# Kernel tuning notes

Measured on AMD Instinct MI355X. Metric: run time of the kernel, lower is better.

The kernel has to match this reference:

```python
import jax, jax.numpy as jnp
import numpy as np

G, NPG = 8192, 8            # graphs, nodes per graph (8 sensors, recon head = 8*9)
N = G * NPG                 # 65536 total nodes
IN, HID, HEADS = 9, 64, 4
NEG_SLOPE = 0.2


def _fc_edges():
    # directed fully-connected edges (no self loops) within each 8-node graph
    i, j = np.meshgrid(np.arange(NPG), np.arange(NPG), indexing='ij')
    m = i != j
    src_l, dst_l = i[m], j[m]                       # 56 edges per graph
    off = (np.arange(G) * NPG)[:, None]
    src = (off + src_l[None, :]).ravel()
    dst = (off + dst_l[None, :]).ravel()
    return np.stack([src, dst]).astype(np.int32)    # [2, 458752]


def setup_inputs() -> dict:
    key = jax.random.key(0)
    ks = jax.random.split(key, 30)
    ei = jnp.asarray(_fc_edges())
    E = ei.shape[1]
    p = lambda k, shape, s=0.1: jax.random.normal(ks[k], shape, jnp.float32) * s
    return {
        'x': jax.random.normal(ks[0], (N, IN), jnp.float32),
        'edge_index': ei,
        'edge_weight': jax.random.uniform(ks[1], (E,), jnp.float32),
        'batch': jnp.repeat(jnp.arange(G, dtype=jnp.int32), NPG),
        'W1': p(2, (IN, HEADS * HID)), 'a_src1': p(3, (HEADS, HID)),
        'a_dst1': p(4, (HEADS, HID)), 'We1': p(5, (1, HEADS * HID)),
        'a_e1': p(6, (HEADS, HID)), 'b1': jnp.zeros((HEADS * HID,), jnp.float32),
        'W2': p(7, (HEADS * HID, HID)), 'a_src2': p(8, (1, HID)),
        'a_dst2': p(9, (1, HID)), 'We2': p(10, (1, HID)),
        'a_e2': p(11, (1, HID)), 'b2': jnp.zeros((HID,), jnp.float32),
        # recon head: 64 -> 128 -> 72
        'Wr1': p(12, (HID, 2 * HID)), 'br1': jnp.zeros((2 * HID,), jnp.float32),
        'Wr2': p(13, (2 * HID, 8 * IN)), 'br2': jnp.zeros((8 * IN,), jnp.float32),
        # classify head: 64 -> 32 -> 1
        'Wc1': p(14, (HID, 32)), 'bc1': jnp.zeros((32,), jnp.float32),
        'Wc2': p(15, (32, 1)), 'bc2': jnp.zeros((1,), jnp.float32),
    }


def _gat_conv(x, edge_index, edge_attr, W, a_src, a_dst, We, a_e, bias):
    """PyG GATConv (eval mode): add_self_loops(fill='mean'), edge_dim features."""
    n = x.shape[0]
    heads, ch = a_src.shape
    src, dst = edge_index[0], edge_index[1]
    # self loops with edge_attr = mean of incoming edge_attr per node
    deg = jax.ops.segment_sum(jnp.ones_like(edge_attr[:, :1]), dst, num_segments=n)
    loop_attr = jax.ops.segment_sum(edge_attr, dst, num_segments=n) / jnp.maximum(deg, 1.0)
    src = jnp.concatenate([src, jnp.arange(n, dtype=src.dtype)])
    dst = jnp.concatenate([dst, jnp.arange(n, dtype=dst.dtype)])
    ea = jnp.concatenate([edge_attr, loop_attr], axis=0)          # [E+N, 1]
    xp = (x @ W).reshape(n, heads, ch)                            # [N, H, C]
    al_s = jnp.einsum('nhc,hc->nh', xp, a_src)
    al_d = jnp.einsum('nhc,hc->nh', xp, a_dst)
    ep = (ea @ We).reshape(-1, heads, ch)                         # [E+N, H, C]
    al_e = jnp.einsum('ehc,hc->eh', ep, a_e)
    alpha = al_s[src] + al_d[dst] + al_e                          # [E+N, H]
    alpha = jax.nn.leaky_relu(alpha, NEG_SLOPE)
    # segment softmax over destination nodes
    m = jax.ops.segment_max(alpha, dst, num_segments=n)
    alpha = jnp.exp(alpha - m[dst])
    s = jax.ops.segment_sum(alpha, dst, num_segments=n)
    alpha = alpha / (s[dst] + 1e-16)
    # scatter-aggregate weighted messages
    out = jax.ops.segment_sum(xp[src] * alpha[..., None], dst, num_segments=n)
    return out.reshape(n, heads * ch) + bias


def reference(x, edge_index, edge_weight, batch,
              W1, a_src1, a_dst1, We1, a_e1, b1,
              W2, a_src2, a_dst2, We2, a_e2, b2,
              Wr1, br1, Wr2, br2, Wc1, bc1, Wc2, bc2):
    ew = edge_weight[:, None]
    h = _gat_conv(x, edge_index, ew, W1, a_src1, a_dst1, We1, a_e1, b1)
    h = jax.nn.elu(h)
    h = _gat_conv(h, edge_index, ew, W2, a_src2, a_dst2, We2, a_e2, b2)
    h = jax.nn.elu(h)
    # global mean pool over graphs
    g = G
    cnt = jax.ops.segment_sum(jnp.ones((h.shape[0], 1), h.dtype), batch, num_segments=g)
    emb = jax.ops.segment_sum(h, batch, num_segments=g) / jnp.maximum(cnt, 1.0)
    recon = jax.nn.relu(emb @ Wr1 + br1) @ Wr2 + br2
    cls = jax.nn.relu(emb @ Wc1 + bc1) @ Wc2 + bc2
    return recon, cls
```

## Files before the change

### kernel.cpp

```cpp
#include <hip/hip_runtime.h>
#include <math.h>

#define NEG 0.2f
#define GROUPS 8192

typedef unsigned short u16;
typedef u16 ushort8 __attribute__((ext_vector_type(8)));
typedef short s16x8 __attribute__((ext_vector_type(8)));
typedef float f32x4 __attribute__((ext_vector_type(4)));

__device__ __forceinline__ float lrelu(float x){ return x >= 0.f ? x : NEG*x; }
__device__ __forceinline__ float eluf(float x){ return x > 0.f ? x : __expf(x) - 1.f; }
__device__ __forceinline__ int eidx(int s,int d){ return s*7 + (d<s ? d : d-1); }
__device__ __forceinline__ float bf2f(u16 u){
    union { unsigned i; float f; } v; v.i = ((unsigned)u)<<16; return v.f;
}
__device__ __forceinline__ u16 f2bf(float f){
    union { float f; unsigned i; } v; v.f = f;
    unsigned r = v.i + 0x7fffu + ((v.i>>16)&1u);
    return (u16)(r>>16);
}

__global__ __launch_bounds__(64)
void prep(const float* __restrict__ W1, const float* __restrict__ a_src1,
          const float* __restrict__ a_dst1, const float* __restrict__ W2,
          const float* __restrict__ Wr1, const float* __restrict__ Wr2,
          const float* __restrict__ Wc1,
          const float* __restrict__ We1, const float* __restrict__ a_e1,
          const float* __restrict__ We2, const float* __restrict__ a_e2,
          u16* __restrict__ wfrag, u16* __restrict__ wr1f,
          u16* __restrict__ wr2f, u16* __restrict__ wc1f,
          float* __restrict__ w1s, float* __restrict__ ces)
{
    const int b = blockIdx.x, l = threadIdx.x;
    const int c0 = l & 15, o = l >> 4;
    if (b < 32) {
        const int t = b >> 3, s = b & 7;
        ushort8 p;
#pragma unroll
        for (int j = 0; j < 8; ++j) p[j] = f2bf(W2[(s*32 + o*8 + j)*64 + t*16 + c0]);
        *(ushort8*)(wfrag + (size_t)(b*64 + l)*8) = p;
    } else if (b < 48) {
        const int f = b - 32, ks = f >> 3, t = f & 7;
        ushort8 p;
#pragma unroll
        for (int j = 0; j < 8; ++j) p[j] = f2bf(Wr1[(ks*32 + o*8 + j)*128 + t*16 + c0]);
        *(ushort8*)(wr1f + (size_t)(f*64 + l)*8) = p;
    } else if (b < 68) {
        const int f = b - 48, ks = f / 5, t = f % 5;
        const int c = t*16 + c0;
        ushort8 p;
#pragma unroll
        for (int j = 0; j < 8; ++j)
            p[j] = (c < 72) ? f2bf(Wr2[(ks*32 + o*8 + j)*72 + c]) : (u16)0;
        *(ushort8*)(wr2f + (size_t)(f*64 + l)*8) = p;
    } else if (b < 72) {
        const int f = b - 68, ks = f >> 1, t = f & 1;
        ushort8 p;
#pragma unroll
        for (int j = 0; j < 8; ++j) p[j] = f2bf(Wc1[(ks*32 + o*8 + j)*32 + t*16 + c0]);
        *(ushort8*)(wc1f + (size_t)(f*64 + l)*8) = p;
    } else if (b == 72) {
        for (int idx = l; idx < 72; idx += 64) {
            const int k = idx >> 3, cc = idx & 7, h = cc & 3;
            const float* av = (cc < 4) ? a_src1 : a_dst1;
            float acc = 0.f;
#pragma unroll 8
            for (int i = 0; i < 64; ++i) acc = fmaf(W1[k*256 + h*64 + i], av[h*64 + i], acc);
            w1s[idx] = acc;
        }
    } else {
        if (l < 4) {
            float c = 0.f;
#pragma unroll 8
            for (int i = 0; i < 64; ++i) c = fmaf(We1[l*64+i], a_e1[l*64+i], c);
            ces[l] = c;
        } else if (l == 4) {
            float c = 0.f;
#pragma unroll 8
            for (int i = 0; i < 64; ++i) c = fmaf(We2[i], a_e2[i], c);
            ces[4] = c;
        }
    }
}

__global__ __launch_bounds__(64, 4)
void gat_fused4(const float* __restrict__ x, const float* __restrict__ ew_g,
    const float* __restrict__ W1, const float* __restrict__ b1,
    const float* __restrict__ a_src2, const float* __restrict__ a_dst2,
    const float* __restrict__ b2,
    const float* __restrict__ br1, const float* __restrict__ br2,
    const float* __restrict__ bc1, const float* __restrict__ Wc2,
    const float* __restrict__ bc2,
    const u16* __restrict__ wfrag, const u16* __restrict__ wr1f,
    const u16* __restrict__ wr2f, const u16* __restrict__ wc1f,
    const float* __restrict__ w1s, const float* __restrict__ cesg,
    float* __restrict__ recon, float* __restrict__ cls)
{
    __shared__ __align__(16) u16 act[2][8][264];
    __shared__ __align__(16) float alpha1[2][4][8][8];
    __shared__ float als1[64], ald1[64];
    __shared__ float als2[2][8], ald2[2][8];
    __shared__ float alpha2[2][8][8];
    __shared__ float xw[2][72];
    __shared__ float ews2[2][56];
    __shared__ float lws[2][8];
    __shared__ float w1sL[72];
    __shared__ __align__(16) u16 embs16[2][64];
    __shared__ __align__(16) u16 r1s16[2][128];
    __shared__ float cesL[6];

    const int lane = threadIdx.x;
    const int n    = lane >> 3;
    const int cg   = lane & 7;
    const int g0   = blockIdx.x * 2;

    {
        const float* xg = x + (size_t)g0 * 72;
        for (int i = lane; i < 144; i += 64) (&xw[0][0])[i] = xg[i];
        const float* eg = ew_g + (size_t)g0 * 56;
        for (int i = lane; i < 112; i += 64) (&ews2[0][0])[i] = eg[i];
        for (int i = lane; i < 72; i += 64) w1sL[i] = w1s[i];
        if (lane < 6) cesL[lane] = cesg[lane];
    }
    __syncthreads();

    if (lane < 16) {
        const int g = lane >> 3, d = lane & 7;
        float s = 0.f;
#pragma unroll
        for (int ss = 0; ss < 8; ++ss) if (ss != d) s += ews2[g][eidx(ss, d)];
        lws[g][d] = s * (1.f/7.f);
    }

    {
        const int gg = lane >> 5, nn = (lane >> 2) & 7, hh = lane & 3;
        float s = 0.f, d = 0.f;
#pragma unroll
        for (int k = 0; k < 9; ++k) {
            const float xv = xw[gg][nn*9 + k];
            s = fmaf(xv, w1sL[k*8 + hh], s);
            d = fmaf(xv, w1sL[k*8 + 4 + hh], d);
        }
        als1[lane] = s; ald1[lane] = d;
    }

    {
        float xr0[9], xr1[9];
#pragma unroll
        for (int k = 0; k < 9; ++k) { xr0[k] = xw[0][n*9+k]; xr1[k] = xw[1][n*9+k]; }
#pragma unroll
        for (int u = 0; u < 4; ++u) {
            const int cb = u*64 + cg*8;
            float a0[8] = {0,0,0,0,0,0,0,0}, a1[8] = {0,0,0,0,0,0,0,0};
#pragma unroll
            for (int k = 0; k < 9; ++k) {
                const float4 w0 = *(const float4*)(W1 + k*256 + cb);
                const float4 w1 = *(const float4*)(W1 + k*256 + cb + 4);
                const float f0 = xr0[k], f1 = xr1[k];
                a0[0]=fmaf(f0,w0.x,a0[0]); a0[1]=fmaf(f0,w0.y,a0[1]);
                a0[2]=fmaf(f0,w0.z,a0[2]); a0[3]=fmaf(f0,w0.w,a0[3]);
                a0[4]=fmaf(f0,w1.x,a0[4]); a0[5]=fmaf(f0,w1.y,a0[5]);
                a0[6]=fmaf(f0,w1.z,a0[6]); a0[7]=fmaf(f0,w1.w,a0[7]);
                a1[0]=fmaf(f1,w0.x,a1[0]); a1[1]=fmaf(f1,w0.y,a1[1]);
                a1[2]=fmaf(f1,w0.z,a1[2]); a1[3]=fmaf(f1,w0.w,a1[3]);
                a1[4]=fmaf(f1,w1.x,a1[4]); a1[5]=fmaf(f1,w1.y,a1[5]);
                a1[6]=fmaf(f1,w1.z,a1[6]); a1[7]=fmaf(f1,w1.w,a1[7]);
            }
            ushort8 p0, p1;
#pragma unroll
            for (int j = 0; j < 8; ++j) { p0[j] = f2bf(a0[j]); p1[j] = f2bf(a1[j]); }
            *(ushort8*)&act[0][n][cb] = p0;
            *(ushort8*)&act[1][n][cb] = p1;
        }
    }
    __syncthreads();

    {
        const int gg = lane >> 5, dd = (lane >> 2) & 7, hh = lane & 3;
        const float ce = cesL[hh], ad = ald1[gg*32 + dd*4 + hh];
        float lg[8], mx = -1e30f;
#pragma unroll
        for (int ss = 0; ss < 8; ++ss) {
            const float w = (ss == dd) ? lws[gg][dd] : ews2[gg][eidx(ss, dd)];
            float t = als1[gg*32 + ss*4 + hh] + ad + ce * w;
            t = lrelu(t);
            lg[ss] = t; mx = fmaxf(mx, t);
        }
        float sum = 0.f;
#pragma unroll
        for (int ss = 0; ss < 8; ++ss) { lg[ss] = __expf(lg[ss] - mx); sum += lg[ss]; }
        const float inv = 1.f / (sum + 1e-16f);
#pragma unroll
        for (int ss = 0; ss < 8; ++ss) alpha1[gg][hh][dd][ss] = lg[ss] * inv;
    }
    __syncthreads();

    for (int g = 0; g < 2; ++g) {
        float hv[32];
#pragma unroll
        for (int u = 0; u < 4; ++u) {
            const float4 al0 = *(const float4*)&alpha1[g][u][n][0];
            const float4 al1 = *(const float4*)&alpha1[g][u][n][4];
            float acc[8] = {0,0,0,0,0,0,0,0};
#pragma unroll
            for (int s = 0; s < 8; ++s) {
                const float av = (s==0)?al0.x:(s==1)?al0.y:(s==2)?al0.z:(s==3)?al0.w:
                                 (s==4)?al1.x:(s==5)?al1.y:(s==6)?al1.z:al1.w;
                const ushort8 v = *(const ushort8*)&act[g][s][u*64 + cg*8];
#pragma unroll
                for (int j = 0; j < 8; ++j) acc[j] = fmaf(av, bf2f(v[j]), acc[j]);
            }
#pragma unroll
            for (int j = 0; j < 8; ++j) hv[u*8+j] = acc[j];
        }
        __syncthreads();
#pragma unroll
        for (int u = 0; u < 4; ++u) {
            const int cb = u*64 + cg*8;
            const float4 b0 = *(const float4*)(b1 + cb);
            const float4 b2v = *(const float4*)(b1 + cb + 4);
            ushort8 p;
            p[0]=f2bf(eluf(hv[u*8+0]+b0.x)); p[1]=f2bf(eluf(hv[u*8+1]+b0.y));
            p[2]=f2bf(eluf(hv[u*8+2]+b0.z)); p[3]=f2bf(eluf(hv[u*8+3]+b0.w));
            p[4]=f2bf(eluf(hv[u*8+4]+b2v.x)); p[5]=f2bf(eluf(hv[u*8+5]+b2v.y));
            p[6]=f2bf(eluf(hv[u*8+6]+b2v.z)); p[7]=f2bf(eluf(hv[u*8+7]+b2v.w));
            *(ushort8*)&act[g][n][cb] = p;
        }
        __syncthreads();
    }

    f32x4 acc[4] = {{0,0,0,0},{0,0,0,0},{0,0,0,0},{0,0,0,0}};
    {
        const int r = lane & 15;
        const u16* arow = &act[r >> 3][r & 7][(lane >> 4) * 8];
#pragma unroll
        for (int s = 0; s < 8; ++s) {
            const s16x8 af = *(const s16x8*)(arow + s * 32);
#pragma unroll
            for (int t = 0; t < 4; ++t) {
                const s16x8 bf = *(const s16x8*)(wfrag + (size_t)(((t*8 + s)*64 + lane))*8);
                acc[t] = __builtin_amdgcn_mfma_f32_16x16x32_bf16(af, bf, acc[t], 0, 0, 0);
            }
        }
    }

    {
        const int c0 = lane & 15;
        float sp[4] = {0,0,0,0}, dp[4] = {0,0,0,0};
#pragma unroll
        for (int t = 0; t < 4; ++t) {
            const float as_ = a_src2[t*16 + c0];
            const float ad_ = a_dst2[t*16 + c0];
#pragma unroll
            for (int i = 0; i < 4; ++i) {
                sp[i] = fmaf(acc[t][i], as_, sp[i]);
                dp[i] = fmaf(acc[t][i], ad_, dp[i]);
            }
        }
#pragma unroll
        for (int i = 0; i < 4; ++i) {
            sp[i] += __shfl_xor(sp[i],1); sp[i] += __shfl_xor(sp[i],2);
            sp[i] += __shfl_xor(sp[i],4); sp[i] += __shfl_xor(sp[i],8);
            dp[i] += __shfl_xor(dp[i],1); dp[i] += __shfl_xor(dp[i],2);
            dp[i] += __shfl_xor(dp[i],4); dp[i] += __shfl_xor(dp[i],8);
        }
        if ((lane & 15) == 0) {
            const int rb = (lane >> 4) * 4;
#pragma unroll
            for (int i = 0; i < 4; ++i) {
                const int r = rb + i;
                als2[r >> 3][r & 7] = sp[i];
                ald2[r >> 3][r & 7] = dp[i];
            }
        }
    }
    __syncthreads();

    float* xf0 = reinterpret_cast<float*>(&act[0][0][0]);
    float* xf1 = reinterpret_cast<float*>(&act[1][0][0]);
    {
        const int c0 = lane & 15;
#pragma unroll
        for (int t = 0; t < 4; ++t)
#pragma unroll
            for (int i = 0; i < 4; ++i) {
                const int r = (lane >> 4)*4 + i;
                float* xf = (r >> 3) ? xf1 : xf0;
                xf[(r & 7)*68 + t*16 + c0] = acc[t][i];
            }
    }
    __syncthreads();

    if (lane < 16) {
        const int g = lane >> 3, d = lane & 7;
        const float ce = cesL[4], ad = ald2[g][d];
        float lg[8], mx = -1e30f;
#pragma unroll
        for (int ss = 0; ss < 8; ++ss) {
            const float w = (ss == d) ? lws[g][d] : ews2[g][eidx(ss, d)];
            float t = als2[g][ss] + ad + ce * w;
            t = lrelu(t);
            lg[ss] = t; mx = fmaxf(mx, t);
        }
        float sum = 0.f;
#pragma unroll
        for (int ss = 0; ss < 8; ++ss) { lg[ss] = __expf(lg[ss] - mx); sum += lg[ss]; }
        const float inv = 1.f / (sum + 1e-16f);
#pragma unroll
        for (int ss = 0; ss < 8; ++ss) alpha2[g][d][ss] = lg[ss] * inv;
    }
    __syncthreads();

    float h2[2][8];
#pragma unroll
    for (int g = 0; g < 2; ++g) {
        const float* xf = g ? xf1 : xf0;
        float a[8] = {0,0,0,0,0,0,0,0};
#pragma unroll
        for (int ss = 0; ss < 8; ++ss) {
            const float av = alpha2[g][n][ss];
            const float4 v0 = *(const float4*)(xf + ss*68 + cg*8);
            const float4 v1 = *(const float4*)(xf + ss*68 + cg*8 + 4);
            a[0]=fmaf(av,v0.x,a[0]); a[1]=fmaf(av,v0.y,a[1]);
            a[2]=fmaf(av,v0.z,a[2]); a[3]=fmaf(av,v0.w,a[3]);
            a[4]=fmaf(av,v1.x,a[4]); a[5]=fmaf(av,v1.y,a[5]);
            a[6]=fmaf(av,v1.z,a[6]); a[7]=fmaf(av,v1.w,a[7]);
        }
        const float4 b0 = *(const float4*)(b2 + cg*8);
        const float4 b1v = *(const float4*)(b2 + cg*8 + 4);
        h2[g][0]=eluf(a[0]+b0.x); h2[g][1]=eluf(a[1]+b0.y);
        h2[g][2]=eluf(a[2]+b0.z); h2[g][3]=eluf(a[3]+b0.w);
        h2[g][4]=eluf(a[4]+b1v.x); h2[g][5]=eluf(a[5]+b1v.y);
        h2[g][6]=eluf(a[6]+b1v.z); h2[g][7]=eluf(a[7]+b1v.w);
    }
#pragma unroll
    for (int g = 0; g < 2; ++g)
#pragma unroll
        for (int j = 0; j < 8; ++j) {
            float v = h2[g][j];
            v += __shfl_xor(v, 8); v += __shfl_xor(v, 16); v += __shfl_xor(v, 32);
            h2[g][j] = v * 0.125f;
        }
    if (n == 0) {
#pragma unroll
        for (int g = 0; g < 2; ++g) {
            ushort8 p;
#pragma unroll
            for (int j = 0; j < 8; ++j) p[j] = f2bf(h2[g][j]);
            *(ushort8*)&embs16[g][lane*8] = p;
        }
    }
    __syncthreads();

    s16x8 aemb0 = {0,0,0,0,0,0,0,0}, aemb1 = {0,0,0,0,0,0,0,0};
    {
        const int r = lane & 15, o = lane >> 4;
        if (r < 2) {
            aemb0 = *(const s16x8*)&embs16[r][o*8];
            aemb1 = *(const s16x8*)&embs16[r][32 + o*8];
        }
    }
    {
        f32x4 ar[8];
        const f32x4 z = {0,0,0,0};
#pragma unroll
        for (int t = 0; t < 8; ++t) ar[t] = z;
#pragma unroll
        for (int t = 0; t < 8; ++t) {
            ar[t] = __builtin_amdgcn_mfma_f32_16x16x32_bf16(
                aemb0, *(const s16x8*)(wr1f + (size_t)((0*8 + t)*64 + lane)*8), ar[t], 0,0,0);
            ar[t] = __builtin_amdgcn_mfma_f32_16x16x32_bf16(
                aemb1, *(const s16x8*)(wr1f + (size_t)((1*8 + t)*64 + lane)*8), ar[t], 0,0,0);
        }
        const int c0 = lane & 15, o = lane >> 4;
        if (o == 0) {
#pragma unroll
            for (int t = 0; t < 8; ++t) {
                const float bb = br1[t*16 + c0];
                r1s16[0][t*16 + c0] = f2bf(fmaxf(ar[t][0] + bb, 0.f));
                r1s16[1][t*16 + c0] = f2bf(fmaxf(ar[t][1] + bb, 0.f));
            }
        }
    }
    __syncthreads();

    {
        f32x4 ac[5];
        const f32x4 z = {0,0,0,0};
#pragma unroll
        for (int t = 0; t < 5; ++t) ac[t] = z;
        const int r = lane & 15, o = lane >> 4;
#pragma unroll
        for (int ks = 0; ks < 4; ++ks) {
            s16x8 a = {0,0,0,0,0,0,0,0};
            if (r < 2) a = *(const s16x8*)&r1s16[r][ks*32 + o*8];
#pragma unroll
            for (int t = 0; t < 5; ++t)
                ac[t] = __builtin_amdgcn_mfma_f32_16x16x32_bf16(
                    a, *(const s16x8*)(wr2f + (size_t)((ks*5 + t)*64 + lane)*8), ac[t], 0,0,0);
        }
        if (o == 0) {
            const int c0 = r;
#pragma unroll
            for (int t = 0; t < 5; ++t) {
                const int c = t*16 + c0;
                if (c < 72) {
                    const float bb = br2[c];
                    recon[(size_t)g0*72 + c]       = ac[t][0] + bb;
                    recon[(size_t)(g0+1)*72 + c]   = ac[t][1] + bb;
                }
            }
        }
    }

    {
        f32x4 ac[2];
        const f32x4 z = {0,0,0,0};
        ac[0] = z; ac[1] = z;
#pragma unroll
        for (int t = 0; t < 2; ++t) {
            ac[t] = __builtin_amdgcn_mfma_f32_16x16x32_bf16(
                aemb0, *(const s16x8*)(wc1f + (size_t)((0*2 + t)*64 + lane)*8), ac[t], 0,0,0);
            ac[t] = __builtin_amdgcn_mfma_f32_16x16x32_bf16(
                aemb1, *(const s16x8*)(wc1f + (size_t)((1*2 + t)*64 + lane)*8), ac[t], 0,0,0);
        }
        const int c0 = lane & 15;
        const float bb0 = bc1[c0], bb1 = bc1[16 + c0];
        const float wc0 = Wc2[c0], wc1v = Wc2[16 + c0];
        float p0 = fmaxf(ac[0][0] + bb0, 0.f)*wc0 + fmaxf(ac[1][0] + bb1, 0.f)*wc1v;
        float p1 = fmaxf(ac[0][1] + bb0, 0.f)*wc0 + fmaxf(ac[1][1] + bb1, 0.f)*wc1v;
        p0 += __shfl_xor(p0,1); p0 += __shfl_xor(p0,2); p0 += __shfl_xor(p0,4); p0 += __shfl_xor(p0,8);
        p1 += __shfl_xor(p1,1); p1 += __shfl_xor(p1,2); p1 += __shfl_xor(p1,4); p1 += __shfl_xor(p1,8);
        if (lane == 0) { cls[g0] = p0 + bc2[0]; cls[g0+1] = p1 + bc2[0]; }
    }
}

extern "C" void kernel_launch(void* const* d_in, const int* in_sizes, int n_in,
                              void* d_out, int out_size, void* d_ws, size_t ws_size,
                              hipStream_t stream) {
    const float* x      = (const float*)d_in[0];
    const float* ew     = (const float*)d_in[2];
    const float* W1     = (const float*)d_in[4];
    const float* a_src1 = (const float*)d_in[5];
    const float* a_dst1 = (const float*)d_in[6];
    const float* We1    = (const float*)d_in[7];
    const float* a_e1   = (const float*)d_in[8];
    const float* b1     = (const float*)d_in[9];
    const float* W2     = (const float*)d_in[10];
    const float* a_src2 = (const float*)d_in[11];
    const float* a_dst2 = (const float*)d_in[12];
    const float* We2    = (const float*)d_in[13];
    const float* a_e2   = (const float*)d_in[14];
    const float* b2     = (const float*)d_in[15];
    const float* Wr1    = (const float*)d_in[16];
    const float* br1    = (const float*)d_in[17];
    const float* Wr2    = (const float*)d_in[18];
    const float* br2    = (const float*)d_in[19];
    const float* Wc1    = (const float*)d_in[20];
    const float* bc1    = (const float*)d_in[21];
    const float* Wc2    = (const float*)d_in[22];
    const float* bc2    = (const float*)d_in[23];

    float* recon = (float*)d_out;
    float* cls   = (float*)d_out + (size_t)GROUPS * 72;

    char* ws = (char*)d_ws;
    u16*   wfrag = (u16*)(ws + 0);
    u16*   wr1f  = (u16*)(ws + 32768);
    u16*   wr2f  = (u16*)(ws + 49152);
    u16*   wc1f  = (u16*)(ws + 69632);
    float* w1s   = (float*)(ws + 73728);
    float* ces   = (float*)(ws + 74016);

    hipLaunchKernelGGL(prep, dim3(74), dim3(64), 0, stream,
                       W1, a_src1, a_dst1, W2, Wr1, Wr2, Wc1,
                       We1, a_e1, We2, a_e2,
                       wfrag, wr1f, wr2f, wc1f, w1s, ces);

    hipLaunchKernelGGL(gat_fused4, dim3(GROUPS/2), dim3(64), 0, stream,
                       x, ew, W1, b1, a_src2, a_dst2, b2,
                       br1, br2, bc1, Wc2, bc2,
                       wfrag, wr1f, wr2f, wc1f, w1s, ces,
                       recon, cls);
}
```

Before: 49.70 us.

## Replace block barriers with LDS waitcnt fences and keep stage data in registers

Since each block is a single 64-lane wavefront, every __syncthreads is replaced by an inline s_waitcnt lgkmcnt(0) fence that also acts as a compiler memory barrier. Node features and the layer-1 attention source/destination scores now stay in registers, read straight from global memory, and neighbour scores are exchanged with __shfl instead of LDS arrays. The embedding and recon-head scratch buffers are aliased onto the alpha buffer to shrink shared memory. Each node's features are now loaded twice from global, and correctness depends on a block never holding more than one wave.

```diff
diff --git a/kernel.cpp b/kernel.cpp
--- a/kernel.cpp
+++ b/kernel.cpp
@@ -8,6 +8,8 @@
 typedef u16 ushort8 __attribute__((ext_vector_type(8)));
 typedef short s16x8 __attribute__((ext_vector_type(8)));
 typedef float f32x4 __attribute__((ext_vector_type(4)));
+
+#define WFENCE() asm volatile("s_waitcnt lgkmcnt(0)" ::: "memory")
 
 __device__ __forceinline__ float lrelu(float x){ return x >= 0.f ? x : NEG*x; }
 __device__ __forceinline__ float eluf(float x){ return x > 0.f ? x : __expf(x) - 1.f; }
@@ -85,7 +87,7 @@
 }
 
 __global__ __launch_bounds__(64, 4)
-void gat_fused4(const float* __restrict__ x, const float* __restrict__ ew_g,
+void gat_fused5(const float* __restrict__ x, const float* __restrict__ ew_g,
     const float* __restrict__ W1, const float* __restrict__ b1,
     const float* __restrict__ a_src2, const float* __restrict__ a_dst2,
     const float* __restrict__ b2,
@@ -98,17 +100,14 @@
     float* __restrict__ recon, float* __restrict__ cls)
 {
     __shared__ __align__(16) u16 act[2][8][264];
-    __shared__ __align__(16) float alpha1[2][4][8][8];
-    __shared__ float als1[64], ald1[64];
+    __shared__ __align__(16) float alpha1f[2][4][8][8];
     __shared__ float als2[2][8], ald2[2][8];
     __shared__ float alpha2[2][8][8];
-    __shared__ float xw[2][72];
     __shared__ float ews2[2][56];
     __shared__ float lws[2][8];
-    __shared__ float w1sL[72];
-    __shared__ __align__(16) u16 embs16[2][64];
-    __shared__ __align__(16) u16 r1s16[2][128];
-    __shared__ float cesL[6];
+
+    u16* const embs16 = (u16*)alpha1f;
+    u16* const r1s16  = (u16*)alpha1f + 128;
 
     const int lane = threadIdx.x;
     const int n    = lane >> 3;
@@ -116,14 +115,31 @@
     const int g0   = blockIdx.x * 2;
 
     {
-        const float* xg = x + (size_t)g0 * 72;
-        for (int i = lane; i < 144; i += 64) (&xw[0][0])[i] = xg[i];
         const float* eg = ew_g + (size_t)g0 * 56;
         for (int i = lane; i < 112; i += 64) (&ews2[0][0])[i] = eg[i];
-        for (int i = lane; i < 72; i += 64) w1sL[i] = w1s[i];
-        if (lane < 6) cesL[lane] = cesg[lane];
-    }
-    __syncthreads();
+    }
+
+    float xr0[9], xr1[9];
+    {
+        const float* p0 = x + (size_t)g0 * 72 + n * 9;
+        const float* p1 = p0 + 72;
+#pragma unroll
+        for (int k = 0; k < 9; ++k) { xr0[k] = p0[k]; xr1[k] = p1[k]; }
+    }
+
+    float alsv = 0.f, aldv = 0.f;
+    {
+        const int gg = lane >> 5, nn = (lane >> 2) & 7, hh = lane & 3;
+        const float* xs = x + (size_t)(g0 + gg) * 72 + nn * 9;
+#pragma unroll
+        for (int k = 0; k < 9; ++k) {
+            const float xv = xs[k];
+            alsv = fmaf(xv, w1s[k*8 + hh], alsv);
+            aldv = fmaf(xv, w1s[k*8 + 4 + hh], aldv);
+        }
+    }
+
+    WFENCE();
 
     if (lane < 16) {
         const int g = lane >> 3, d = lane & 7;
@@ -134,21 +150,6 @@
     }
 
     {
-        const int gg = lane >> 5, nn = (lane >> 2) & 7, hh = lane & 3;
-        float s = 0.f, d = 0.f;
-#pragma unroll
-        for (int k = 0; k < 9; ++k) {
-            const float xv = xw[gg][nn*9 + k];
-            s = fmaf(xv, w1sL[k*8 + hh], s);
-            d = fmaf(xv, w1sL[k*8 + 4 + hh], d);
-        }
-        als1[lane] = s; ald1[lane] = d;
-    }
-
-    {
-        float xr0[9], xr1[9];
-#pragma unroll
-        for (int k = 0; k < 9; ++k) { xr0[k] = xw[0][n*9+k]; xr1[k] = xw[1][n*9+k]; }
 #pragma unroll
         for (int u = 0; u < 4; ++u) {
             const int cb = u*64 + cg*8;
@@ -174,16 +175,19 @@
             *(ushort8*)&act[1][n][cb] = p1;
         }
     }
-    __syncthreads();
+
+    WFENCE();
 
     {
         const int gg = lane >> 5, dd = (lane >> 2) & 7, hh = lane & 3;
-        const float ce = cesL[hh], ad = ald1[gg*32 + dd*4 + hh];
+        const float ce = cesg[hh];
+        const float ad = aldv;
         float lg[8], mx = -1e30f;
 #pragma unroll
         for (int ss = 0; ss < 8; ++ss) {
+            const float as_ = __shfl(alsv, (lane & 0x23) | (ss << 2));
             const float w = (ss == dd) ? lws[gg][dd] : ews2[gg][eidx(ss, dd)];
-            float t = als1[gg*32 + ss*4 + hh] + ad + ce * w;
+            float t = as_ + ad + ce * w;
             t = lrelu(t);
             lg[ss] = t; mx = fmaxf(mx, t);
         }
@@ -192,16 +196,17 @@
         for (int ss = 0; ss < 8; ++ss) { lg[ss] = __expf(lg[ss] - mx); sum += lg[ss]; }
         const float inv = 1.f / (sum + 1e-16f);
 #pragma unroll
-        for (int ss = 0; ss < 8; ++ss) alpha1[gg][hh][dd][ss] = lg[ss] * inv;
-    }
-    __syncthreads();
+        for (int ss = 0; ss < 8; ++ss) alpha1f[gg][hh][dd][ss] = lg[ss] * inv;
+    }
+
+    WFENCE();
 
     for (int g = 0; g < 2; ++g) {
         float hv[32];
 #pragma unroll
         for (int u = 0; u < 4; ++u) {
-            const float4 al0 = *(const float4*)&alpha1[g][u][n][0];
-            const float4 al1 = *(const float4*)&alpha1[g][u][n][4];
+            const float4 al0 = *(const float4*)&alpha1f[g][u][n][0];
+            const float4 al1 = *(const float4*)&alpha1f[g][u][n][4];
             float acc[8] = {0,0,0,0,0,0,0,0};
 #pragma unroll
             for (int s = 0; s < 8; ++s) {
@@ -214,7 +219,7 @@
 #pragma unroll
             for (int j = 0; j < 8; ++j) hv[u*8+j] = acc[j];
         }
-        __syncthreads();
+        WFENCE();
 #pragma unroll
         for (int u = 0; u < 4; ++u) {
             const int cb = u*64 + cg*8;
@@ -227,7 +232,7 @@
             p[6]=f2bf(eluf(hv[u*8+6]+b2v.z)); p[7]=f2bf(eluf(hv[u*8+7]+b2v.w));
             *(ushort8*)&act[g][n][cb] = p;
         }
-        __syncthreads();
+        WFENCE();
     }
 
     f32x4 acc[4] = {{0,0,0,0},{0,0,0,0},{0,0,0,0},{0,0,0,0}};
@@ -275,7 +280,7 @@
             }
         }
     }
-    __syncthreads();
+    WFENCE();
 
     float* xf0 = reinterpret_cast<float*>(&act[0][0][0]);
     float* xf1 = reinterpret_cast<float*>(&act[1][0][0]);
@@ -290,11 +295,11 @@
                 xf[(r & 7)*68 + t*16 + c0] = acc[t][i];
             }
     }
-    __syncthreads();
+    WFENCE();
 
     if (lane < 16) {
         const int g = lane >> 3, d = lane & 7;
-        const float ce = cesL[4], ad = ald2[g][d];
+        const float ce = cesg[4], ad = ald2[g][d];
         float lg[8], mx = -1e30f;
 #pragma unroll
         for (int ss = 0; ss < 8; ++ss) {
@@ -310,7 +315,7 @@
 #pragma unroll
         for (int ss = 0; ss < 8; ++ss) alpha2[g][d][ss] = lg[ss] * inv;
     }
-    __syncthreads();
+    WFENCE();
 
     float h2[2][8];
 #pragma unroll
@@ -348,17 +353,17 @@
             ushort8 p;
 #pragma unroll
             for (int j = 0; j < 8; ++j) p[j] = f2bf(h2[g][j]);
-            *(ushort8*)&embs16[g][lane*8] = p;
-        }
-    }
-    __syncthreads();
+            *(ushort8*)&embs16[g*64 + lane*8] = p;
+        }
+    }
+    WFENCE();
 
     s16x8 aemb0 = {0,0,0,0,0,0,0,0}, aemb1 = {0,0,0,0,0,0,0,0};
     {
         const int r = lane & 15, o = lane >> 4;
         if (r < 2) {
-            aemb0 = *(const s16x8*)&embs16[r][o*8];
-            aemb1 = *(const s16x8*)&embs16[r][32 + o*8];
+            aemb0 = *(const s16x8*)&embs16[r*64 + o*8];
+            aemb1 = *(const s16x8*)&embs16[r*64 + 32 + o*8];
         }
     }
     {
@@ -378,12 +383,12 @@
 #pragma unroll
             for (int t = 0; t < 8; ++t) {
                 const float bb = br1[t*16 + c0];
-                r1s16[0][t*16 + c0] = f2bf(fmaxf(ar[t][0] + bb, 0.f));
-                r1s16[1][t*16 + c0] = f2bf(fmaxf(ar[t][1] + bb, 0.f));
-            }
-        }
-    }
-    __syncthreads();
+                r1s16[0*128 + t*16 + c0] = f2bf(fmaxf(ar[t][0] + bb, 0.f));
+                r1s16[1*128 + t*16 + c0] = f2bf(fmaxf(ar[t][1] + bb, 0.f));
+            }
+        }
+    }
+    WFENCE();
 
     {
         f32x4 ac[5];
@@ -394,7 +399,7 @@
 #pragma unroll
         for (int ks = 0; ks < 4; ++ks) {
             s16x8 a = {0,0,0,0,0,0,0,0};
-            if (r < 2) a = *(const s16x8*)&r1s16[r][ks*32 + o*8];
+            if (r < 2) a = *(const s16x8*)&r1s16[r*128 + ks*32 + o*8];
 #pragma unroll
             for (int t = 0; t < 5; ++t)
                 ac[t] = __builtin_amdgcn_mfma_f32_16x16x32_bf16(
@@ -478,7 +483,7 @@
                        We1, a_e1, We2, a_e2,
                        wfrag, wr1f, wr2f, wc1f, w1s, ces);
 
-    hipLaunchKernelGGL(gat_fused4, dim3(GROUPS/2), dim3(64), 0, stream,
+    hipLaunchKernelGGL(gat_fused5, dim3(GROUPS/2), dim3(64), 0, stream,
                        x, ew, W1, b1, a_src2, a_dst2, b2,
                        br1, br2, bc1, Wc2, bc2,
                        wfrag, wr1f, wr2f, wc1f, w1s, ces,
```

After: 54.93 us. 10.5% more time.

## Aggregate raw inputs before W1 projection and build MFMA operands in registers

Applied to the files above, without the earlier changes.

Layer-1 attention aggregation now runs on the 9-dim raw features (alpha·x) before the W1 projection, using linearity, instead of projecting to 256 channels and then aggregating. The projected, biased and ELU-activated layer-1 output is built directly in registers as the MFMA A operand for the layer-2 matmul. This removes the large bf16 activation buffer in shared memory and several barriers. Each lane now recomputes its 8-channel W1 slice (9×8 FMAs per k-step) and reads W1 from global memory. Alpha is stored as bf16, which adds a small precision change.

```diff
diff --git a/kernel.cpp b/kernel.cpp
--- a/kernel.cpp
+++ b/kernel.cpp
@@ -85,7 +85,7 @@
 }
 
 __global__ __launch_bounds__(64, 4)
-void gat_fused4(const float* __restrict__ x, const float* __restrict__ ew_g,
+void gat_fused8(const float* __restrict__ x, const float* __restrict__ ew_g,
     const float* __restrict__ W1, const float* __restrict__ b1,
     const float* __restrict__ a_src2, const float* __restrict__ a_dst2,
     const float* __restrict__ b2,
@@ -97,23 +97,26 @@
     const float* __restrict__ w1s, const float* __restrict__ cesg,
     float* __restrict__ recon, float* __restrict__ cls)
 {
-    __shared__ __align__(16) u16 act[2][8][264];
-    __shared__ __align__(16) float alpha1[2][4][8][8];
+    __shared__ __align__(16) float xw[2][72];
+    __shared__ float ews2[2][56];
+    __shared__ float lws[2][8];
+    __shared__ float w1sL[72];
+    __shared__ float cesL[6];
+    __shared__ __align__(16) u16 alpha1b[2][4][8][8];
     __shared__ float als1[64], ald1[64];
     __shared__ float als2[2][8], ald2[2][8];
     __shared__ float alpha2[2][8][8];
-    __shared__ float xw[2][72];
-    __shared__ float ews2[2][56];
-    __shared__ float lws[2][8];
-    __shared__ float w1sL[72];
+    __shared__ __align__(16) float xp2f[2][8][68];
     __shared__ __align__(16) u16 embs16[2][64];
     __shared__ __align__(16) u16 r1s16[2][128];
-    __shared__ float cesL[6];
 
     const int lane = threadIdx.x;
     const int n    = lane >> 3;
     const int cg   = lane & 7;
     const int g0   = blockIdx.x * 2;
+    const int o    = lane >> 4;
+    const int rr   = lane & 15;
+    const int gA   = rr >> 3, nA = rr & 7;
 
     {
         const float* xg = x + (size_t)g0 * 72;
@@ -144,36 +147,6 @@
         }
         als1[lane] = s; ald1[lane] = d;
     }
-
-    {
-        float xr0[9], xr1[9];
-#pragma unroll
-        for (int k = 0; k < 9; ++k) { xr0[k] = xw[0][n*9+k]; xr1[k] = xw[1][n*9+k]; }
-#pragma unroll
-        for (int u = 0; u < 4; ++u) {
-            const int cb = u*64 + cg*8;
-            float a0[8] = {0,0,0,0,0,0,0,0}, a1[8] = {0,0,0,0,0,0,0,0};
-#pragma unroll
-            for (int k = 0; k < 9; ++k) {
-                const float4 w0 = *(const float4*)(W1 + k*256 + cb);
-                const float4 w1 = *(const float4*)(W1 + k*256 + cb + 4);
-                const float f0 = xr0[k], f1 = xr1[k];
-                a0[0]=fmaf(f0,w0.x,a0[0]); a0[1]=fmaf(f0,w0.y,a0[1]);
-                a0[2]=fmaf(f0,w0.z,a0[2]); a0[3]=fmaf(f0,w0.w,a0[3]);
-                a0[4]=fmaf(f0,w1.x,a0[4]); a0[5]=fmaf(f0,w1.y,a0[5]);
-                a0[6]=fmaf(f0,w1.z,a0[6]); a0[7]=fmaf(f0,w1.w,a0[7]);
-                a1[0]=fmaf(f1,w0.x,a1[0]); a1[1]=fmaf(f1,w0.y,a1[1]);
-                a1[2]=fmaf(f1,w0.z,a1[2]); a1[3]=fmaf(f1,w0.w,a1[3]);
-                a1[4]=fmaf(f1,w1.x,a1[4]); a1[5]=fmaf(f1,w1.y,a1[5]);
-                a1[6]=fmaf(f1,w1.z,a1[6]); a1[7]=fmaf(f1,w1.w,a1[7]);
-            }
-            ushort8 p0, p1;
-#pragma unroll
-            for (int j = 0; j < 8; ++j) { p0[j] = f2bf(a0[j]); p1[j] = f2bf(a1[j]); }
-            *(ushort8*)&act[0][n][cb] = p0;
-            *(ushort8*)&act[1][n][cb] = p1;
-        }
-    }
     __syncthreads();
 
     {
@@ -191,57 +164,66 @@
 #pragma unroll
         for (int ss = 0; ss < 8; ++ss) { lg[ss] = __expf(lg[ss] - mx); sum += lg[ss]; }
         const float inv = 1.f / (sum + 1e-16f);
-#pragma unroll
-        for (int ss = 0; ss < 8; ++ss) alpha1[gg][hh][dd][ss] = lg[ss] * inv;
-    }
-    __syncthreads();
-
-    for (int g = 0; g < 2; ++g) {
-        float hv[32];
-#pragma unroll
-        for (int u = 0; u < 4; ++u) {
-            const float4 al0 = *(const float4*)&alpha1[g][u][n][0];
-            const float4 al1 = *(const float4*)&alpha1[g][u][n][4];
-            float acc[8] = {0,0,0,0,0,0,0,0};
-#pragma unroll
-            for (int s = 0; s < 8; ++s) {
-                const float av = (s==0)?al0.x:(s==1)?al0.y:(s==2)?al0.z:(s==3)?al0.w:
-                                 (s==4)?al1.x:(s==5)?al1.y:(s==6)?al1.z:al1.w;
-                const ushort8 v = *(const ushort8*)&act[g][s][u*64 + cg*8];
-#pragma unroll
-                for (int j = 0; j < 8; ++j) acc[j] = fmaf(av, bf2f(v[j]), acc[j]);
-            }
-#pragma unroll
-            for (int j = 0; j < 8; ++j) hv[u*8+j] = acc[j];
-        }
-        __syncthreads();
-#pragma unroll
-        for (int u = 0; u < 4; ++u) {
-            const int cb = u*64 + cg*8;
-            const float4 b0 = *(const float4*)(b1 + cb);
-            const float4 b2v = *(const float4*)(b1 + cb + 4);
-            ushort8 p;
-            p[0]=f2bf(eluf(hv[u*8+0]+b0.x)); p[1]=f2bf(eluf(hv[u*8+1]+b0.y));
-            p[2]=f2bf(eluf(hv[u*8+2]+b0.z)); p[3]=f2bf(eluf(hv[u*8+3]+b0.w));
-            p[4]=f2bf(eluf(hv[u*8+4]+b2v.x)); p[5]=f2bf(eluf(hv[u*8+5]+b2v.y));
-            p[6]=f2bf(eluf(hv[u*8+6]+b2v.z)); p[7]=f2bf(eluf(hv[u*8+7]+b2v.w));
-            *(ushort8*)&act[g][n][cb] = p;
-        }
-        __syncthreads();
+        ushort8 ap;
+#pragma unroll
+        for (int ss = 0; ss < 8; ++ss) ap[ss] = f2bf(lg[ss] * inv);
+        *(ushort8*)&alpha1b[gg][hh][dd][0] = ap;
+    }
+    __syncthreads();
+
+    float y[4][9];
+    {
+        float af[4][8];
+#pragma unroll
+        for (int h = 0; h < 4; ++h) {
+            const ushort8 a8 = *(const ushort8*)&alpha1b[gA][h][nA][0];
+#pragma unroll
+            for (int s = 0; s < 8; ++s) af[h][s] = bf2f(a8[s]);
+        }
+#pragma unroll
+        for (int k = 0; k < 9; ++k) {
+            float xk[8];
+#pragma unroll
+            for (int s = 0; s < 8; ++s) xk[s] = xw[gA][s*9 + k];
+#pragma unroll
+            for (int h = 0; h < 4; ++h) {
+                float a = 0.f;
+#pragma unroll
+                for (int s = 0; s < 8; ++s) a = fmaf(af[h][s], xk[s], a);
+                y[h][k] = a;
+            }
+        }
     }
 
     f32x4 acc[4] = {{0,0,0,0},{0,0,0,0},{0,0,0,0},{0,0,0,0}};
-    {
-        const int r = lane & 15;
-        const u16* arow = &act[r >> 3][r & 7][(lane >> 4) * 8];
-#pragma unroll
-        for (int s = 0; s < 8; ++s) {
-            const s16x8 af = *(const s16x8*)(arow + s * 32);
-#pragma unroll
-            for (int t = 0; t < 4; ++t) {
-                const s16x8 bf = *(const s16x8*)(wfrag + (size_t)(((t*8 + s)*64 + lane))*8);
-                acc[t] = __builtin_amdgcn_mfma_f32_16x16x32_bf16(af, bf, acc[t], 0, 0, 0);
-            }
+#pragma unroll
+    for (int s = 0; s < 8; ++s) {
+        const int h = s >> 1;
+        const int cb = s*32 + o*8;
+        float v[8];
+        {
+            const float4 bb0 = *(const float4*)(b1 + cb);
+            const float4 bb1 = *(const float4*)(b1 + cb + 4);
+            v[0]=bb0.x; v[1]=bb0.y; v[2]=bb0.z; v[3]=bb0.w;
+            v[4]=bb1.x; v[5]=bb1.y; v[6]=bb1.z; v[7]=bb1.w;
+        }
+#pragma unroll
+        for (int k = 0; k < 9; ++k) {
+            const float4 w0 = *(const float4*)(W1 + k*256 + cb);
+            const float4 w1 = *(const float4*)(W1 + k*256 + cb + 4);
+            const float yv = y[h][k];
+            v[0]=fmaf(yv,w0.x,v[0]); v[1]=fmaf(yv,w0.y,v[1]);
+            v[2]=fmaf(yv,w0.z,v[2]); v[3]=fmaf(yv,w0.w,v[3]);
+            v[4]=fmaf(yv,w1.x,v[4]); v[5]=fmaf(yv,w1.y,v[5]);
+            v[6]=fmaf(yv,w1.z,v[6]); v[7]=fmaf(yv,w1.w,v[7]);
+        }
+        s16x8 A;
+#pragma unroll
+        for (int j = 0; j < 8; ++j) A[j] = (short)f2bf(eluf(v[j]));
+#pragma unroll
+        for (int t = 0; t < 4; ++t) {
+            const s16x8 bf = *(const s16x8*)(wfrag + (size_t)(((t*8 + s)*64 + lane))*8);
+            acc[t] = __builtin_amdgcn_mfma_f32_16x16x32_bf16(A, bf, acc[t], 0, 0, 0);
         }
     }
 
@@ -266,7 +248,7 @@
             dp[i] += __shfl_xor(dp[i],4); dp[i] += __shfl_xor(dp[i],8);
         }
         if ((lane & 15) == 0) {
-            const int rb = (lane >> 4) * 4;
+            const int rb = o * 4;
 #pragma unroll
             for (int i = 0; i < 4; ++i) {
                 const int r = rb + i;
@@ -275,19 +257,15 @@
             }
         }
     }
-    __syncthreads();
-
-    float* xf0 = reinterpret_cast<float*>(&act[0][0][0]);
-    float* xf1 = reinterpret_cast<float*>(&act[1][0][0]);
+
     {
         const int c0 = lane & 15;
 #pragma unroll
         for (int t = 0; t < 4; ++t)
 #pragma unroll
             for (int i = 0; i < 4; ++i) {
-                const int r = (lane >> 4)*4 + i;
-                float* xf = (r >> 3) ? xf1 : xf0;
-                xf[(r & 7)*68 + t*16 + c0] = acc[t][i];
+                const int r = o*4 + i;
+                xp2f[r >> 3][r & 7][t*16 + c0] = acc[t][i];
             }
     }
     __syncthreads();
@@ -315,7 +293,7 @@
     float h2[2][8];
 #pragma unroll
     for (int g = 0; g < 2; ++g) {
-        const float* xf = g ? xf1 : xf0;
+        const float* xf = &xp2f[g][0][0];
         float a[8] = {0,0,0,0,0,0,0,0};
 #pragma unroll
         for (int ss = 0; ss < 8; ++ss) {
@@ -355,7 +333,7 @@
 
     s16x8 aemb0 = {0,0,0,0,0,0,0,0}, aemb1 = {0,0,0,0,0,0,0,0};
     {
-        const int r = lane & 15, o = lane >> 4;
+        const int r = lane & 15;
         if (r < 2) {
             aemb0 = *(const s16x8*)&embs16[r][o*8];
             aemb1 = *(const s16x8*)&embs16[r][32 + o*8];
@@ -373,7 +351,7 @@
             ar[t] = __builtin_amdgcn_mfma_f32_16x16x32_bf16(
                 aemb1, *(const s16x8*)(wr1f + (size_t)((1*8 + t)*64 + lane)*8), ar[t], 0,0,0);
         }
-        const int c0 = lane & 15, o = lane >> 4;
+        const int c0 = lane & 15;
         if (o == 0) {
 #pragma unroll
             for (int t = 0; t < 8; ++t) {
@@ -390,7 +368,7 @@
         const f32x4 z = {0,0,0,0};
 #pragma unroll
         for (int t = 0; t < 5; ++t) ac[t] = z;
-        const int r = lane & 15, o = lane >> 4;
+        const int r = lane & 15;
 #pragma unroll
         for (int ks = 0; ks < 4; ++ks) {
             s16x8 a = {0,0,0,0,0,0,0,0};
@@ -478,7 +456,7 @@
                        We1, a_e1, We2, a_e2,
                        wfrag, wr1f, wr2f, wc1f, w1s, ces);
 
-    hipLaunchKernelGGL(gat_fused4, dim3(GROUPS/2), dim3(64), 0, stream,
+    hipLaunchKernelGGL(gat_fused8, dim3(GROUPS/2), dim3(64), 0, stream,
                        x, ew, W1, b1, a_src2, a_dst2, b2,
                        br1, br2, bc1, Wc2, bc2,
                        wfrag, wr1f, wr2f, wc1f, w1s, ces,
```

Result: slower. 52.83 us (+6.3%).
